# Kernel tuning notes

Hardware: AMD Instinct MI355X
Metric: run time of the kernel (lower is better)

## Reference

```python
import jax, jax.numpy as jnp
import numpy as np

HIDDEN = 1024
HEADS = 16
HEAD_DIM = HIDDEN // HEADS

def setup_inputs() -> dict:
    key = jax.random.key(0)
    ks = jax.random.split(key, 11)
    B, T, D = 2, 2048, HIDDEN
    s = 1.0 / np.sqrt(D)
    return {
        "query": jax.random.normal(ks[0], (B, T, D), jnp.float32),
        "key": jax.random.normal(ks[1], (B, T, D), jnp.float32),
        "value": jax.random.normal(ks[2], (B, T, D), jnp.float32),
        "Wq": jax.random.normal(ks[3], (D, D), jnp.float32) * s,
        "bq": jnp.zeros((D,), jnp.float32),
        "Wk": jax.random.normal(ks[4], (D, D), jnp.float32) * s,
        "bk": jnp.zeros((D,), jnp.float32),
        "Wv": jax.random.normal(ks[5], (D, D), jnp.float32) * s,
        "bv": jnp.zeros((D,), jnp.float32),
        "Wo": jax.random.normal(ks[6], (D, D), jnp.float32) * s,
        "bo": jnp.zeros((D,), jnp.float32),
    }

def reference(query, key, value, Wq, bq, Wk, bk, Wv, bv, Wo, bo):
    B, Tq, D = query.shape
    Tk = key.shape[1]
    H, Hd = HEADS, HEAD_DIM
    # projections -> [B, H, T, Hd]
    Q = (query @ Wq + bq).reshape(B, Tq, H, Hd).transpose(0, 2, 1, 3)
    K = (key @ Wk + bk).reshape(B, Tk, H, Hd).transpose(0, 2, 1, 3)
    V = (value @ Wv + bv).reshape(B, Tk, H, Hd).transpose(0, 2, 1, 3)
    scale = jnp.sqrt(jnp.asarray(Hd, Q.dtype))
    scores = jnp.einsum('bhqd,bhkd->bhqk', Q, K) / scale  # [B,H,Tq,Tk]
    causal = jnp.triu(jnp.ones((Tq, Tk), bool), k=1)
    scores = jnp.where(causal[None, None], jnp.asarray(-jnp.inf, scores.dtype), scores)
    attn = jax.nn.softmax(scores, axis=-1)
    out = jnp.einsum('bhqk,bhkd->bhqd', attn, V)  # [B,H,Tq,Hd]
    out = out.transpose(0, 2, 1, 3).reshape(B, Tq, D)
    return out @ Wo + bo
```

## Files before the change

### kernel.cpp

```cpp
#include <hip/hip_runtime.h>
#include <hip/hip_bf16.h>


typedef __bf16 bf16_t;
typedef __bf16 bf16x8 __attribute__((ext_vector_type(8)));
typedef __bf16 bf16x4 __attribute__((ext_vector_type(4)));
typedef __bf16 bf16x2 __attribute__((ext_vector_type(2)));
typedef short short4v __attribute__((ext_vector_type(4)));
typedef float f32x4 __attribute__((ext_vector_type(4)));
typedef unsigned int u32;

#define D_MODEL 1024
#define SEQ_T   2048
#define NHEAD   16
#define HDIM    64
#define M_ROWS  4096
#define MEGA    (1024 * 1024)

__device__ __forceinline__ void gl2lds16(const void* g, void* l) {
    __builtin_amdgcn_global_load_lds((const __attribute__((address_space(1))) u32*)g,
                                     (__attribute__((address_space(3))) u32*)l, 16, 0, 0);
}

__device__ __forceinline__ short4v as_s4(bf16x4 v) {
    union { bf16x4 h; short4v s; } u; u.h = v; return u.s;
}

__global__ __launch_bounds__(256) void prep(
    const float* __restrict__ Wq, const float* __restrict__ Wk,
    const float* __restrict__ Wv, const float* __restrict__ Wo,
    const float* __restrict__ Xq, const float* __restrict__ Xk, const float* __restrict__ Xv,
    bf16_t* __restrict__ Wqt, bf16_t* __restrict__ Wkt,
    bf16_t* __restrict__ Wvt, bf16_t* __restrict__ Wot,
    bf16_t* __restrict__ Xb)
{
    int blk = blockIdx.x, tid = threadIdx.x;
    if (blk < 4096) {
        int wi = blk >> 10, t = blk & 1023;
        int n0 = (t & 31) * 32, k0 = (t >> 5) * 32;
        const float* W = wi == 0 ? Wq : (wi == 1 ? Wk : (wi == 2 ? Wv : Wo));
        bf16_t* Wt = wi == 0 ? Wqt : (wi == 1 ? Wkt : (wi == 2 ? Wvt : Wot));
        __shared__ float tile[32][33];
        int tx = tid & 31, ty = tid >> 5;
#pragma unroll
        for (int i = 0; i < 32; i += 8)
            tile[ty + i][tx] = W[(k0 + ty + i) * D_MODEL + n0 + tx];
        __syncthreads();
#pragma unroll
        for (int i = 0; i < 32; i += 8)
            Wt[(size_t)(n0 + ty + i) * D_MODEL + k0 + tx] = (bf16_t)tile[tx][ty + i];
    } else {
        int b2 = blk - 4096;
        int xi = b2 >> 10;
        const float* X = xi == 0 ? Xq : (xi == 1 ? Xk : Xv);
        bf16_t* XB = Xb + (size_t)xi * M_ROWS * D_MODEL;
        size_t base = (size_t)(b2 & 1023) * 4096 + tid * 16;
        const float4* xp = (const float4*)(X + base);
        float4 a0 = xp[0], a1 = xp[1], a2 = xp[2], a3 = xp[3];
        bf16x8 o0, o1;
        o0[0] = (bf16_t)a0.x; o0[1] = (bf16_t)a0.y; o0[2] = (bf16_t)a0.z; o0[3] = (bf16_t)a0.w;
        o0[4] = (bf16_t)a1.x; o0[5] = (bf16_t)a1.y; o0[6] = (bf16_t)a1.z; o0[7] = (bf16_t)a1.w;
        o1[0] = (bf16_t)a2.x; o1[1] = (bf16_t)a2.y; o1[2] = (bf16_t)a2.z; o1[3] = (bf16_t)a2.w;
        o1[4] = (bf16_t)a3.x; o1[5] = (bf16_t)a3.y; o1[6] = (bf16_t)a3.z; o1[7] = (bf16_t)a3.w;
        *(bf16x8*)(XB + base) = o0;
        *(bf16x8*)(XB + base + 8) = o1;
    }
}

template <bool PRECAST>
__global__ __launch_bounds__(256) void proj_fused(
    const float* __restrict__ Xq, const float* __restrict__ Xk, const float* __restrict__ Xv,
    const bf16_t* __restrict__ Xb,
    const bf16_t* __restrict__ Wqt, const bf16_t* __restrict__ Wkt, const bf16_t* __restrict__ Wvt,
    const float* __restrict__ bq, const float* __restrict__ bk, const float* __restrict__ bv,
    bf16_t* __restrict__ Qh, bf16_t* __restrict__ Kh, bf16_t* __restrict__ Vt)
{
    __shared__ bf16_t Ab[128 * 64];
    __shared__ bf16_t Bb[128 * 64];
    int tid = threadIdx.x;
    int w = tid >> 6, lane = tid & 63, lo16 = lane & 15, quad = lane >> 4;
    int m0 = blockIdx.x * 128;
    int proj = blockIdx.y >> 3;
    int n0 = (blockIdx.y & 7) * 128;
    const float*  X    = proj == 0 ? Xq  : (proj == 1 ? Xk  : Xv);
    const bf16_t* XB   = Xb + (size_t)proj * M_ROWS * D_MODEL;
    const bf16_t* Wt   = proj == 0 ? Wqt : (proj == 1 ? Wkt : Wvt);
    const float*  bias = proj == 0 ? bq  : (proj == 1 ? bk  : bv);
    int wm = (w >> 1) * 64, wn = (w & 1) * 64;

    f32x4 acc[4][4];
#pragma unroll
    for (int i = 0; i < 4; i++)
#pragma unroll
        for (int j = 0; j < 4; j++) acc[i][j] = (f32x4){0.f, 0.f, 0.f, 0.f};

    for (int k0 = 0; k0 < D_MODEL; k0 += 64) {
        __syncthreads();
#pragma unroll
        for (int p = 0; p < 4; p++) {
            int idx = p * 256 + tid;
            int row = idx >> 3, cp = idx & 7, cl = (cp - row) & 7;
            if (PRECAST) {
                gl2lds16(XB + (size_t)(m0 + row) * D_MODEL + k0 + cl * 8, Ab + idx * 8);
            } else {
                const float* as = X + (size_t)(m0 + row) * D_MODEL + k0 + cl * 8;
                float4 a0 = *(const float4*)as, a1 = *(const float4*)(as + 4);
                bf16x8 av;
                av[0] = (bf16_t)a0.x; av[1] = (bf16_t)a0.y; av[2] = (bf16_t)a0.z; av[3] = (bf16_t)a0.w;
                av[4] = (bf16_t)a1.x; av[5] = (bf16_t)a1.y; av[6] = (bf16_t)a1.z; av[7] = (bf16_t)a1.w;
                *(bf16x8*)(Ab + idx * 8) = av;
            }
            gl2lds16(Wt + (size_t)(n0 + row) * D_MODEL + k0 + cl * 8, Bb + idx * 8);
        }
        __syncthreads();
#pragma unroll
        for (int kh = 0; kh < 2; kh++) {
            bf16x8 af[4], bfr[4];
#pragma unroll
            for (int i = 0; i < 4; i++) {
                int row = wm + i * 16 + lo16;
                af[i] = *(bf16x8*)(Ab + row * 64 + (((kh * 4 + quad) + row) & 7) * 8);
            }
#pragma unroll
            for (int j = 0; j < 4; j++) {
                int row = wn + j * 16 + lo16;
                bfr[j] = *(bf16x8*)(Bb + row * 64 + (((kh * 4 + quad) + row) & 7) * 8);
            }
#pragma unroll
            for (int i = 0; i < 4; i++)
#pragma unroll
                for (int j = 0; j < 4; j++)
                    acc[i][j] = __builtin_amdgcn_mfma_f32_16x16x32_bf16(af[i], bfr[j], acc[i][j], 0, 0, 0);
        }
    }

    float qscale = proj == 0 ? 0.125f : 1.0f;
#pragma unroll
    for (int j = 0; j < 4; j++) {
        int col = n0 + wn + j * 16 + lo16;
        float bv2 = bias[col];
        int h = col >> 6, hd = col & 63;
#pragma unroll
        for (int i = 0; i < 4; i++) {
#pragma unroll
            for (int r = 0; r < 4; r++) {
                int m = m0 + wm + i * 16 + quad * 4 + r;
                int b = m >> 11, t = m & 2047;
                bf16_t val = (bf16_t)((acc[i][j][r] + bv2) * qscale);
                if (proj == 2)
                    Vt[(((size_t)(b * NHEAD + h) * HDIM + hd) * SEQ_T) + t] = val;
                else if (proj == 1)
                    Kh[(((size_t)(b * NHEAD + h) * SEQ_T + t) * HDIM) + hd] = val;
                else
                    Qh[(((size_t)(b * NHEAD + h) * SEQ_T + t) * HDIM) + hd] = val;
            }
        }
    }
}

__global__ __launch_bounds__(128) void flash_attn(const bf16_t* __restrict__ Qh,
                                                  const bf16_t* __restrict__ Kh,
                                                  const bf16_t* __restrict__ Vt,
                                                  bf16_t* __restrict__ Ob) {
    int bh = blockIdx.x & 31;
    int pr = blockIdx.x >> 5;
    int tid = threadIdx.x;
    int w = tid >> 6, lane = tid & 63, lo16 = lane & 15, quad = lane >> 4;

    __shared__ bf16_t KL[64 * 64];
    __shared__ bf16_t VL[64 * 64];

    const bf16_t* Qp = Qh + (size_t)bh * SEQ_T * HDIM;
    const bf16_t* Kp = Kh + (size_t)bh * SEQ_T * HDIM;
    const bf16_t* Vp = Vt + (size_t)bh * HDIM * SEQ_T;
    int b = bh >> 4, h = bh & 15;

#pragma unroll
    for (int u = 0; u < 2; u++) {
        int qt = u == 0 ? (31 - pr) : pr;
        int qbase = qt * 64 + w * 32;

        bf16x8 qf[2][2];
#pragma unroll
        for (int n = 0; n < 2; n++) {
            const bf16_t* qr = Qp + (size_t)(qbase + n * 16 + lo16) * HDIM;
            qf[n][0] = *(const bf16x8*)(qr + quad * 8);
            qf[n][1] = *(const bf16x8*)(qr + 32 + quad * 8);
        }

        f32x4 oacc[2][4];
        float lsum[2] = {0.f, 0.f};
#pragma unroll
        for (int n = 0; n < 2; n++)
#pragma unroll
            for (int t = 0; t < 4; t++) oacc[n][t] = (f32x4){0.f, 0.f, 0.f, 0.f};

        for (int kt = 0; kt <= qt; kt++) {
            __syncthreads();
#pragma unroll
            for (int p = 0; p < 4; p++) {
                int idx = p * 128 + tid;
                int row = idx >> 3, cp = idx & 7, cl = (cp - row) & 7;
                gl2lds16(Kp + (size_t)(kt * 64 + row) * HDIM + cl * 8, (bf16_t*)KL + idx * 8);
                gl2lds16(Vp + (size_t)row * SEQ_T + kt * 64 + cl * 8, (bf16_t*)VL + idx * 8);
            }
            __syncthreads();

            bf16x8 kf[4][2];
#pragma unroll
            for (int s = 0; s < 4; s++) {
                int keyr = s * 16 + lo16;
                kf[s][0] = *(bf16x8*)(KL + keyr * 64 + ((quad + keyr) & 7) * 8);
                kf[s][1] = *(bf16x8*)(KL + keyr * 64 + ((quad + 4 + keyr) & 7) * 8);
            }

            bool diag = (kt == qt);
            short4v pf[2][4];
#pragma unroll
            for (int n = 0; n < 2; n++) {
                f32x4 sacc[4];
#pragma unroll
                for (int s = 0; s < 4; s++) sacc[s] = (f32x4){0.f, 0.f, 0.f, 0.f};
#pragma unroll
                for (int s = 0; s < 4; s++) {
                    sacc[s] = __builtin_amdgcn_mfma_f32_16x16x32_bf16(kf[s][0], qf[n][0], sacc[s], 0, 0, 0);
                    sacc[s] = __builtin_amdgcn_mfma_f32_16x16x32_bf16(kf[s][1], qf[n][1], sacc[s], 0, 0, 0);
                }
                int q = qbase + n * 16 + lo16;
#pragma unroll
                for (int s = 0; s < 4; s++) {
                    bf16x4 pv;
#pragma unroll
                    for (int r = 0; r < 4; r++) {
                        float e = __expf(sacc[s][r]);
                        if (diag) {
                            int key = kt * 64 + s * 16 + quad * 4 + r;
                            e = (key <= q) ? e : 0.f;
                        }
                        lsum[n] += e;
                        pv[r] = (bf16_t)e;
                    }
                    pf[n][s] = as_s4(pv);
                }
            }

#pragma unroll
            for (int t = 0; t < 4; t++) {
                int drow = t * 16 + lo16;
#pragma unroll
                for (int s = 0; s < 4; s++) {
                    int c = s * 16 + quad * 4;
                    int phys = ((c >> 3) + drow) & 7;
                    bf16x4 vf = *(bf16x4*)(VL + drow * 64 + phys * 8 + (c & 7));
                    short4v vfs = as_s4(vf);
                    oacc[0][t] = __builtin_amdgcn_mfma_f32_16x16x16bf16_1k(vfs, pf[0][s], oacc[0][t], 0, 0, 0);
                    oacc[1][t] = __builtin_amdgcn_mfma_f32_16x16x16bf16_1k(vfs, pf[1][s], oacc[1][t], 0, 0, 0);
                }
            }
        }

#pragma unroll
        for (int n = 0; n < 2; n++) {
            float lt = lsum[n];
            lt += __shfl_xor(lt, 16);
            lt += __shfl_xor(lt, 32);
            float inv = 1.f / lt;
            int q = qbase + n * 16 + lo16;
            bf16_t* dst = Ob + ((size_t)b * SEQ_T + q) * D_MODEL + h * HDIM;
#pragma unroll
            for (int t = 0; t < 4; t++) {
#pragma unroll
                for (int rp = 0; rp < 2; rp++) {
                    int d0 = t * 16 + quad * 4 + rp * 2;
                    bf16x2 pk;
                    pk[0] = (bf16_t)(oacc[n][t][rp * 2] * inv);
                    pk[1] = (bf16_t)(oacc[n][t][rp * 2 + 1] * inv);
                    *(bf16x2*)(dst + d0) = pk;
                }
            }
        }
    }
}

__global__ __launch_bounds__(256) void out_gemm(const bf16_t* __restrict__ A,
                                                const bf16_t* __restrict__ Wt,
                                                const float* __restrict__ bias,
                                                float* __restrict__ out) {
    __shared__ bf16_t Ab[128 * 64];
    __shared__ bf16_t Bb[64 * 64];
    int tid = threadIdx.x;
    int w = tid >> 6, lane = tid & 63, lo16 = lane & 15, quad = lane >> 4;
    int m0 = blockIdx.x * 128;
    int n0 = blockIdx.y * 64;
    int wm = (w >> 1) * 64, wn = (w & 1) * 32;

    f32x4 acc[4][2];
#pragma unroll
    for (int i = 0; i < 4; i++)
#pragma unroll
        for (int j = 0; j < 2; j++) acc[i][j] = (f32x4){0.f, 0.f, 0.f, 0.f};

    for (int k0 = 0; k0 < D_MODEL; k0 += 64) {
        __syncthreads();
#pragma unroll
        for (int p = 0; p < 4; p++) {
            int idx = p * 256 + tid;
            int row = idx >> 3, cp = idx & 7, cl = (cp - row) & 7;
            gl2lds16(A + (size_t)(m0 + row) * D_MODEL + k0 + cl * 8, Ab + idx * 8);
        }
#pragma unroll
        for (int p = 0; p < 2; p++) {
            int idx = p * 256 + tid;
            int row = idx >> 3, cp = idx & 7, cl = (cp - row) & 7;
            gl2lds16(Wt + (size_t)(n0 + row) * D_MODEL + k0 + cl * 8, Bb + idx * 8);
        }
        __syncthreads();
#pragma unroll
        for (int kh = 0; kh < 2; kh++) {
            bf16x8 af[4], bfr[2];
#pragma unroll
            for (int i = 0; i < 4; i++) {
                int row = wm + i * 16 + lo16;
                af[i] = *(bf16x8*)(Ab + row * 64 + (((kh * 4 + quad) + row) & 7) * 8);
            }
#pragma unroll
            for (int j = 0; j < 2; j++) {
                int row = wn + j * 16 + lo16;
                bfr[j] = *(bf16x8*)(Bb + row * 64 + (((kh * 4 + quad) + row) & 7) * 8);
            }
#pragma unroll
            for (int i = 0; i < 4; i++)
#pragma unroll
                for (int j = 0; j < 2; j++)
                    acc[i][j] = __builtin_amdgcn_mfma_f32_16x16x32_bf16(af[i], bfr[j], acc[i][j], 0, 0, 0);
        }
    }

#pragma unroll
    for (int j = 0; j < 2; j++) {
        int col = n0 + wn + j * 16 + lo16;
        float bv2 = bias[col];
#pragma unroll
        for (int i = 0; i < 4; i++)
#pragma unroll
            for (int r = 0; r < 4; r++) {
                int m = m0 + wm + i * 16 + quad * 4 + r;
                out[(size_t)m * D_MODEL + col] = acc[i][j][r] + bv2;
            }
    }
}

extern "C" void kernel_launch(void* const* d_in, const int* in_sizes, int n_in,
                              void* d_out, int out_size, void* d_ws, size_t ws_size,
                              hipStream_t stream) {
    const float* q  = (const float*)d_in[0];
    const float* k  = (const float*)d_in[1];
    const float* v  = (const float*)d_in[2];
    const float* Wq = (const float*)d_in[3];
    const float* bq = (const float*)d_in[4];
    const float* Wk = (const float*)d_in[5];
    const float* bk = (const float*)d_in[6];
    const float* Wv = (const float*)d_in[7];
    const float* bv = (const float*)d_in[8];
    const float* Wo = (const float*)d_in[9];
    const float* bo = (const float*)d_in[10];
    float* out = (float*)d_out;

    bf16_t* Wqt = (bf16_t*)d_ws;
    bf16_t* Wkt = Wqt + (size_t)MEGA;
    bf16_t* Wvt = Wkt + (size_t)MEGA;
    bf16_t* Wot = Wvt + (size_t)MEGA;
    bf16_t* Qh  = Wot + (size_t)MEGA;
    bf16_t* Kh  = Qh  + (size_t)M_ROWS * D_MODEL;
    bf16_t* Vt  = Kh  + (size_t)M_ROWS * D_MODEL;
    bf16_t* Xb  = Vt  + (size_t)M_ROWS * D_MODEL;
    bf16_t* Ob  = Xb;

    bool precast = ws_size >= (size_t)(4 * MEGA + 6 * M_ROWS * D_MODEL) * sizeof(bf16_t);

    int prep_blocks = precast ? 4096 + 3 * 1024 : 4096;
    prep<<<prep_blocks, 256, 0, stream>>>(Wq, Wk, Wv, Wo, q, k, v, Wqt, Wkt, Wvt, Wot, Xb);

    dim3 pg(M_ROWS / 128, 24);
    if (precast)
        proj_fused<true><<<pg, 256, 0, stream>>>(q, k, v, Xb, Wqt, Wkt, Wvt, bq, bk, bv, Qh, Kh, Vt);
    else
        proj_fused<false><<<pg, 256, 0, stream>>>(q, k, v, Xb, Wqt, Wkt, Wvt, bq, bk, bv, Qh, Kh, Vt);

    flash_attn<<<32 * 16, 128, 0, stream>>>(Qh, Kh, Vt, Ob);

    dim3 og(M_ROWS / 128, D_MODEL / 64);
    out_gemm<<<og, 256, 0, stream>>>(Ob, Wot, bo, out);
}
```

Baseline: 236.8 us.

## Double-buffer LDS staging in projection, attention and output GEMM kernels

```diff
diff --git a/kernel.cpp b/kernel.cpp
--- a/kernel.cpp
+++ b/kernel.cpp
@@ -75,8 +75,8 @@
     const float* __restrict__ bq, const float* __restrict__ bk, const float* __restrict__ bv,
     bf16_t* __restrict__ Qh, bf16_t* __restrict__ Kh, bf16_t* __restrict__ Vt)
 {
-    __shared__ bf16_t Ab[128 * 64];
-    __shared__ bf16_t Bb[128 * 64];
+    __shared__ bf16_t Ab[2][128 * 64];
+    __shared__ bf16_t Bb[2][128 * 64];
     int tid = threadIdx.x;
     int w = tid >> 6, lane = tid & 63, lo16 = lane & 15, quad = lane >> 4;
     int m0 = blockIdx.x * 128;
@@ -88,43 +88,48 @@
     const float*  bias = proj == 0 ? bq  : (proj == 1 ? bk  : bv);
     int wm = (w >> 1) * 64, wn = (w & 1) * 64;
 
-    f32x4 acc[4][4];
-#pragma unroll
-    for (int i = 0; i < 4; i++)
-#pragma unroll
-        for (int j = 0; j < 4; j++) acc[i][j] = (f32x4){0.f, 0.f, 0.f, 0.f};
-
-    for (int k0 = 0; k0 < D_MODEL; k0 += 64) {
-        __syncthreads();
+    auto stage = [&](int buf, int k0) {
 #pragma unroll
         for (int p = 0; p < 4; p++) {
             int idx = p * 256 + tid;
             int row = idx >> 3, cp = idx & 7, cl = (cp - row) & 7;
             if (PRECAST) {
-                gl2lds16(XB + (size_t)(m0 + row) * D_MODEL + k0 + cl * 8, Ab + idx * 8);
+                gl2lds16(XB + (size_t)(m0 + row) * D_MODEL + k0 + cl * 8, Ab[buf] + idx * 8);
             } else {
                 const float* as = X + (size_t)(m0 + row) * D_MODEL + k0 + cl * 8;
                 float4 a0 = *(const float4*)as, a1 = *(const float4*)(as + 4);
                 bf16x8 av;
                 av[0] = (bf16_t)a0.x; av[1] = (bf16_t)a0.y; av[2] = (bf16_t)a0.z; av[3] = (bf16_t)a0.w;
                 av[4] = (bf16_t)a1.x; av[5] = (bf16_t)a1.y; av[6] = (bf16_t)a1.z; av[7] = (bf16_t)a1.w;
-                *(bf16x8*)(Ab + idx * 8) = av;
-            }
-            gl2lds16(Wt + (size_t)(n0 + row) * D_MODEL + k0 + cl * 8, Bb + idx * 8);
-        }
-        __syncthreads();
+                *(bf16x8*)(Ab[buf] + idx * 8) = av;
+            }
+            gl2lds16(Wt + (size_t)(n0 + row) * D_MODEL + k0 + cl * 8, Bb[buf] + idx * 8);
+        }
+    };
+
+    f32x4 acc[4][4];
+#pragma unroll
+    for (int i = 0; i < 4; i++)
+#pragma unroll
+        for (int j = 0; j < 4; j++) acc[i][j] = (f32x4){0.f, 0.f, 0.f, 0.f};
+
+    stage(0, 0);
+    __syncthreads();
+    for (int it = 0; it < 16; it++) {
+        int cur = it & 1;
+        if (it + 1 < 16) stage(cur ^ 1, (it + 1) * 64);
 #pragma unroll
         for (int kh = 0; kh < 2; kh++) {
             bf16x8 af[4], bfr[4];
 #pragma unroll
             for (int i = 0; i < 4; i++) {
                 int row = wm + i * 16 + lo16;
-                af[i] = *(bf16x8*)(Ab + row * 64 + (((kh * 4 + quad) + row) & 7) * 8);
+                af[i] = *(bf16x8*)(Ab[cur] + row * 64 + (((kh * 4 + quad) + row) & 7) * 8);
             }
 #pragma unroll
             for (int j = 0; j < 4; j++) {
                 int row = wn + j * 16 + lo16;
-                bfr[j] = *(bf16x8*)(Bb + row * 64 + (((kh * 4 + quad) + row) & 7) * 8);
+                bfr[j] = *(bf16x8*)(Bb[cur] + row * 64 + (((kh * 4 + quad) + row) & 7) * 8);
             }
 #pragma unroll
             for (int i = 0; i < 4; i++)
@@ -132,6 +137,7 @@
                 for (int j = 0; j < 4; j++)
                     acc[i][j] = __builtin_amdgcn_mfma_f32_16x16x32_bf16(af[i], bfr[j], acc[i][j], 0, 0, 0);
         }
+        __syncthreads();
     }
 
     float qscale = proj == 0 ? 0.125f : 1.0f;
@@ -167,98 +173,50 @@
     int tid = threadIdx.x;
     int w = tid >> 6, lane = tid & 63, lo16 = lane & 15, quad = lane >> 4;
 
-    __shared__ bf16_t KL[64 * 64];
-    __shared__ bf16_t VL[64 * 64];
+    __shared__ bf16_t KL[2][64 * 64];
+    __shared__ bf16_t VL[2][64 * 64];
 
     const bf16_t* Qp = Qh + (size_t)bh * SEQ_T * HDIM;
     const bf16_t* Kp = Kh + (size_t)bh * SEQ_T * HDIM;
     const bf16_t* Vp = Vt + (size_t)bh * HDIM * SEQ_T;
     int b = bh >> 4, h = bh & 15;
 
-#pragma unroll
-    for (int u = 0; u < 2; u++) {
-        int qt = u == 0 ? (31 - pr) : pr;
-        int qbase = qt * 64 + w * 32;
-
-        bf16x8 qf[2][2];
+    auto stageKV = [&](int buf, int kt) {
+#pragma unroll
+        for (int p = 0; p < 4; p++) {
+            int idx = p * 128 + tid;
+            int row = idx >> 3, cp = idx & 7, cl = (cp - row) & 7;
+            gl2lds16(Kp + (size_t)(kt * 64 + row) * HDIM + cl * 8, KL[buf] + idx * 8);
+            gl2lds16(Vp + (size_t)row * SEQ_T + kt * 64 + cl * 8, VL[buf] + idx * 8);
+        }
+    };
+
+    int qt_hi = 31 - pr, qt_lo = pr;
+    int n0t = qt_hi + 1, ntot = n0t + qt_lo + 1;
+
+    int qt_cur = qt_hi;
+    int qbase = qt_cur * 64 + w * 32;
+    bf16x8 qf[2][2];
+    f32x4 oacc[2][4];
+    float lsum[2];
+
+    auto load_q = [&]() {
 #pragma unroll
         for (int n = 0; n < 2; n++) {
             const bf16_t* qr = Qp + (size_t)(qbase + n * 16 + lo16) * HDIM;
             qf[n][0] = *(const bf16x8*)(qr + quad * 8);
             qf[n][1] = *(const bf16x8*)(qr + 32 + quad * 8);
         }
-
-        f32x4 oacc[2][4];
-        float lsum[2] = {0.f, 0.f};
-#pragma unroll
-        for (int n = 0; n < 2; n++)
+    };
+    auto zero_state = [&]() {
+#pragma unroll
+        for (int n = 0; n < 2; n++) {
+            lsum[n] = 0.f;
 #pragma unroll
             for (int t = 0; t < 4; t++) oacc[n][t] = (f32x4){0.f, 0.f, 0.f, 0.f};
-
-        for (int kt = 0; kt <= qt; kt++) {
-            __syncthreads();
-#pragma unroll
-            for (int p = 0; p < 4; p++) {
-                int idx = p * 128 + tid;
-                int row = idx >> 3, cp = idx & 7, cl = (cp - row) & 7;
-                gl2lds16(Kp + (size_t)(kt * 64 + row) * HDIM + cl * 8, (bf16_t*)KL + idx * 8);
-                gl2lds16(Vp + (size_t)row * SEQ_T + kt * 64 + cl * 8, (bf16_t*)VL + idx * 8);
-            }
-            __syncthreads();
-
-            bf16x8 kf[4][2];
-#pragma unroll
-            for (int s = 0; s < 4; s++) {
-                int keyr = s * 16 + lo16;
-                kf[s][0] = *(bf16x8*)(KL + keyr * 64 + ((quad + keyr) & 7) * 8);
-                kf[s][1] = *(bf16x8*)(KL + keyr * 64 + ((quad + 4 + keyr) & 7) * 8);
-            }
-
-            bool diag = (kt == qt);
-            short4v pf[2][4];
-#pragma unroll
-            for (int n = 0; n < 2; n++) {
-                f32x4 sacc[4];
-#pragma unroll
-                for (int s = 0; s < 4; s++) sacc[s] = (f32x4){0.f, 0.f, 0.f, 0.f};
-#pragma unroll
-                for (int s = 0; s < 4; s++) {
-                    sacc[s] = __builtin_amdgcn_mfma_f32_16x16x32_bf16(kf[s][0], qf[n][0], sacc[s], 0, 0, 0);
-                    sacc[s] = __builtin_amdgcn_mfma_f32_16x16x32_bf16(kf[s][1], qf[n][1], sacc[s], 0, 0, 0);
-                }
-                int q = qbase + n * 16 + lo16;
-#pragma unroll
-                for (int s = 0; s < 4; s++) {
-                    bf16x4 pv;
-#pragma unroll
-                    for (int r = 0; r < 4; r++) {
-                        float e = __expf(sacc[s][r]);
-                        if (diag) {
-                            int key = kt * 64 + s * 16 + quad * 4 + r;
-                            e = (key <= q) ? e : 0.f;
-                        }
-                        lsum[n] += e;
-                        pv[r] = (bf16_t)e;
-                    }
-                    pf[n][s] = as_s4(pv);
-                }
-            }
-
-#pragma unroll
-            for (int t = 0; t < 4; t++) {
-                int drow = t * 16 + lo16;
-#pragma unroll
-                for (int s = 0; s < 4; s++) {
-                    int c = s * 16 + quad * 4;
-                    int phys = ((c >> 3) + drow) & 7;
-                    bf16x4 vf = *(bf16x4*)(VL + drow * 64 + phys * 8 + (c & 7));
-                    short4v vfs = as_s4(vf);
-                    oacc[0][t] = __builtin_amdgcn_mfma_f32_16x16x16bf16_1k(vfs, pf[0][s], oacc[0][t], 0, 0, 0);
-                    oacc[1][t] = __builtin_amdgcn_mfma_f32_16x16x16bf16_1k(vfs, pf[1][s], oacc[1][t], 0, 0, 0);
-                }
-            }
-        }
-
+        }
+    };
+    auto epilogue = [&]() {
 #pragma unroll
         for (int n = 0; n < 2; n++) {
             float lt = lsum[n];
@@ -279,65 +237,144 @@
                 }
             }
         }
-    }
+    };
+
+    load_q();
+    zero_state();
+    stageKV(0, 0);
+    __syncthreads();
+
+    for (int j = 0; j < ntot; j++) {
+        int cur = j & 1;
+        if (j + 1 < ntot) {
+            int jn = j + 1;
+            int ktn = jn < n0t ? jn : jn - n0t;
+            stageKV(jn & 1, ktn);
+        }
+        int kt = j < n0t ? j : j - n0t;
+
+        bf16x8 kf[4][2];
+#pragma unroll
+        for (int s = 0; s < 4; s++) {
+            int keyr = s * 16 + lo16;
+            kf[s][0] = *(bf16x8*)(KL[cur] + keyr * 64 + ((quad + keyr) & 7) * 8);
+            kf[s][1] = *(bf16x8*)(KL[cur] + keyr * 64 + ((quad + 4 + keyr) & 7) * 8);
+        }
+
+        bool diag = (kt == qt_cur);
+        short4v pf[2][4];
+#pragma unroll
+        for (int n = 0; n < 2; n++) {
+            f32x4 sacc[4];
+#pragma unroll
+            for (int s = 0; s < 4; s++) sacc[s] = (f32x4){0.f, 0.f, 0.f, 0.f};
+#pragma unroll
+            for (int s = 0; s < 4; s++) {
+                sacc[s] = __builtin_amdgcn_mfma_f32_16x16x32_bf16(kf[s][0], qf[n][0], sacc[s], 0, 0, 0);
+                sacc[s] = __builtin_amdgcn_mfma_f32_16x16x32_bf16(kf[s][1], qf[n][1], sacc[s], 0, 0, 0);
+            }
+            int q = qbase + n * 16 + lo16;
+#pragma unroll
+            for (int s = 0; s < 4; s++) {
+                bf16x4 pv;
+#pragma unroll
+                for (int r = 0; r < 4; r++) {
+                    float e = __expf(sacc[s][r]);
+                    if (diag) {
+                        int key = kt * 64 + s * 16 + quad * 4 + r;
+                        e = (key <= q) ? e : 0.f;
+                    }
+                    lsum[n] += e;
+                    pv[r] = (bf16_t)e;
+                }
+                pf[n][s] = as_s4(pv);
+            }
+        }
+
+#pragma unroll
+        for (int t = 0; t < 4; t++) {
+            int drow = t * 16 + lo16;
+#pragma unroll
+            for (int s = 0; s < 4; s++) {
+                int c = s * 16 + quad * 4;
+                int phys = ((c >> 3) + drow) & 7;
+                bf16x4 vf = *(bf16x4*)(VL[cur] + drow * 64 + phys * 8 + (c & 7));
+                short4v vfs = as_s4(vf);
+                oacc[0][t] = __builtin_amdgcn_mfma_f32_16x16x16bf16_1k(vfs, pf[0][s], oacc[0][t], 0, 0, 0);
+                oacc[1][t] = __builtin_amdgcn_mfma_f32_16x16x16bf16_1k(vfs, pf[1][s], oacc[1][t], 0, 0, 0);
+            }
+        }
+
+        __syncthreads();
+
+        if (j == n0t - 1) {
+            epilogue();
+            qt_cur = qt_lo;
+            qbase = qt_cur * 64 + w * 32;
+            load_q();
+            zero_state();
+        }
+    }
+    epilogue();
 }
 
 __global__ __launch_bounds__(256) void out_gemm(const bf16_t* __restrict__ A,
                                                 const bf16_t* __restrict__ Wt,
                                                 const float* __restrict__ bias,
                                                 float* __restrict__ out) {
-    __shared__ bf16_t Ab[128 * 64];
-    __shared__ bf16_t Bb[64 * 64];
+    __shared__ bf16_t Ab[2][128 * 64];
+    __shared__ bf16_t Bb[2][128 * 64];
     int tid = threadIdx.x;
     int w = tid >> 6, lane = tid & 63, lo16 = lane & 15, quad = lane >> 4;
     int m0 = blockIdx.x * 128;
-    int n0 = blockIdx.y * 64;
-    int wm = (w >> 1) * 64, wn = (w & 1) * 32;
-
-    f32x4 acc[4][2];
-#pragma unroll
-    for (int i = 0; i < 4; i++)
-#pragma unroll
-        for (int j = 0; j < 2; j++) acc[i][j] = (f32x4){0.f, 0.f, 0.f, 0.f};
-
-    for (int k0 = 0; k0 < D_MODEL; k0 += 64) {
-        __syncthreads();
+    int n0 = blockIdx.y * 128;
+    int wm = (w >> 1) * 64, wn = (w & 1) * 64;
+
+    auto stage = [&](int buf, int k0) {
 #pragma unroll
         for (int p = 0; p < 4; p++) {
             int idx = p * 256 + tid;
             int row = idx >> 3, cp = idx & 7, cl = (cp - row) & 7;
-            gl2lds16(A + (size_t)(m0 + row) * D_MODEL + k0 + cl * 8, Ab + idx * 8);
-        }
-#pragma unroll
-        for (int p = 0; p < 2; p++) {
-            int idx = p * 256 + tid;
-            int row = idx >> 3, cp = idx & 7, cl = (cp - row) & 7;
-            gl2lds16(Wt + (size_t)(n0 + row) * D_MODEL + k0 + cl * 8, Bb + idx * 8);
-        }
-        __syncthreads();
+            gl2lds16(A  + (size_t)(m0 + row) * D_MODEL + k0 + cl * 8, Ab[buf] + idx * 8);
+            gl2lds16(Wt + (size_t)(n0 + row) * D_MODEL + k0 + cl * 8, Bb[buf] + idx * 8);
+        }
+    };
+
+    f32x4 acc[4][4];
+#pragma unroll
+    for (int i = 0; i < 4; i++)
+#pragma unroll
+        for (int j = 0; j < 4; j++) acc[i][j] = (f32x4){0.f, 0.f, 0.f, 0.f};
+
+    stage(0, 0);
+    __syncthreads();
+    for (int it = 0; it < 16; it++) {
+        int cur = it & 1;
+        if (it + 1 < 16) stage(cur ^ 1, (it + 1) * 64);
 #pragma unroll
         for (int kh = 0; kh < 2; kh++) {
-            bf16x8 af[4], bfr[2];
+            bf16x8 af[4], bfr[4];
 #pragma unroll
             for (int i = 0; i < 4; i++) {
                 int row = wm + i * 16 + lo16;
-                af[i] = *(bf16x8*)(Ab + row * 64 + (((kh * 4 + quad) + row) & 7) * 8);
-            }
-#pragma unroll
-            for (int j = 0; j < 2; j++) {
+                af[i] = *(bf16x8*)(Ab[cur] + row * 64 + (((kh * 4 + quad) + row) & 7) * 8);
+            }
+#pragma unroll
+            for (int j = 0; j < 4; j++) {
                 int row = wn + j * 16 + lo16;
-                bfr[j] = *(bf16x8*)(Bb + row * 64 + (((kh * 4 + quad) + row) & 7) * 8);
+                bfr[j] = *(bf16x8*)(Bb[cur] + row * 64 + (((kh * 4 + quad) + row) & 7) * 8);
             }
 #pragma unroll
             for (int i = 0; i < 4; i++)
 #pragma unroll
-                for (int j = 0; j < 2; j++)
+                for (int j = 0; j < 4; j++)
                     acc[i][j] = __builtin_amdgcn_mfma_f32_16x16x32_bf16(af[i], bfr[j], acc[i][j], 0, 0, 0);
         }
-    }
-
-#pragma unroll
-    for (int j = 0; j < 2; j++) {
+        __syncthreads();
+    }
+
+#pragma unroll
+    for (int j = 0; j < 4; j++) {
         int col = n0 + wn + j * 16 + lo16;
         float bv2 = bias[col];
 #pragma unroll
@@ -389,6 +426,6 @@
 
     flash_attn<<<32 * 16, 128, 0, stream>>>(Qh, Kh, Vt, Ob);
 
-    dim3 og(M_ROWS / 128, D_MODEL / 64);
+    dim3 og(M_ROWS / 128, D_MODEL / 128);
     out_gemm<<<og, 256, 0, stream>>>(Ob, Wot, bo, out);
 }
```

Result: slower. 262.6 us (+10.9%).
